# Kernel optimization log

Hardware: AMD Instinct MI355X
Metric: run time of the kernel (lower is better)

## Reference

```python
import jax, jax.numpy as jnp
import numpy as np


def setup_inputs() -> dict:
    key = jax.random.key(0)
    k1, k2, k3 = jax.random.split(key, 3)
    B, S, D, E, H = 4, 2048, 1024, 8, 1024
    x = jax.random.normal(k1, (B, S, D), dtype=jnp.float32)
    Wg = jax.random.normal(k2, (D, E), dtype=jnp.float32) / np.sqrt(D)
    We = jax.random.normal(k3, (E, D, H), dtype=jnp.float32) / np.sqrt(D)
    be = jnp.zeros((E, H), dtype=jnp.float32)
    return {"x": x, "Wg": Wg, "We": We, "be": be}


def reference(x, Wg, We, be):
    B, S, D = x.shape
    E = Wg.shape[1]
    T = B * S
    xf = x.reshape(T, D)
    # Top-2 gating (softmax over experts, renormalize the chosen 2)
    gates = jax.nn.softmax(xf @ Wg, axis=-1)                 # [T, E]
    top_g, top_i = jax.lax.top_k(gates, 2)                   # [T, 2]
    top_g = top_g / jnp.sum(top_g, axis=-1, keepdims=True)
    # Dense dispatch matrix: dispatch[e, t] = combined gate weight of token t for expert e
    tok = jnp.arange(T)
    dispatch = jnp.zeros((E, T), dtype=gates.dtype)
    for i in range(2):  # fixed top-2, not a data loop
        dispatch = dispatch.at[top_i[:, i], tok].add(top_g[:, i])
    # Per-expert linear (grouped GEMM over all tokens), then weighted combine
    y = jnp.einsum('td,edh->eth', xf, We) + be[:, None, :]   # [E, T, H]
    out = jnp.einsum('et,eth->th', dispatch, y)              # [T, H]
    return out.reshape(B, S, -1)
```

## Files before the change

### kernel.cpp

```cpp
#include <hip/hip_runtime.h>
#include <hip/hip_bf16.h>

#define T_TOK 8192
#define DDIM  1024
#define NEXP  8
#define HDIM  1024
#define SLOT_CAP 17536
#define NCBLK 32

typedef short bf16x8 __attribute__((ext_vector_type(8)));
typedef float f32x4  __attribute__((ext_vector_type(4)));

typedef const __attribute__((address_space(1))) unsigned int* gas_ptr;
typedef __attribute__((address_space(3))) unsigned int*       las_ptr;
#define GLD16(gp, lp) __builtin_amdgcn_global_load_lds((gas_ptr)(gp), (las_ptr)(lp), 16, 0, 0)

static __device__ __forceinline__ unsigned short f2b(float f) {
    union { float f; unsigned int u; } v; v.f = f;
    unsigned int u = v.u;
    u += 0x7fffu + ((u >> 16) & 1u);
    return (unsigned short)(u >> 16);
}
static __device__ __forceinline__ float b2f(unsigned short h) {
    union { unsigned int u; float f; } v; v.u = ((unsigned int)h) << 16;
    return v.f;
}

__global__ __launch_bounds__(256) void moe_routing(
    const float* __restrict__ x, const float* __restrict__ wg,
    unsigned short* __restrict__ xb,
    int* __restrict__ tok_e, float* __restrict__ tok_g)
{
    __shared__ double red[256 * 9];
    __shared__ double part[64];
    __shared__ double lf[NEXP];

    int t   = blockIdx.x;
    int tid = threadIdx.x;

    float4 xv = ((const float4*)(x + (size_t)t * DDIM))[tid];
    ushort4 xs;
    xs.x = f2b(xv.x); xs.y = f2b(xv.y); xs.z = f2b(xv.z); xs.w = f2b(xv.w);
    ((ushort4*)(xb + (size_t)t * DDIM))[tid] = xs;

    double s[NEXP];
    #pragma unroll
    for (int e = 0; e < NEXP; e++) s[e] = 0.0;
    const float* wr = wg + (size_t)tid * 4 * NEXP;
    #pragma unroll
    for (int j = 0; j < 4; j++) {
        double xj = (double)((&xv.x)[j]);
        #pragma unroll
        for (int e = 0; e < NEXP; e++)
            s[e] += xj * (double)wr[j * NEXP + e];
    }
    #pragma unroll
    for (int e = 0; e < NEXP; e++) red[tid * 9 + e] = s[e];
    __syncthreads();

    if (tid < 64) {
        int e = tid >> 3, p = tid & 7;
        double acc = 0.0;
        for (int i = 0; i < 32; i++) acc += red[(i * 8 + p) * 9 + e];
        part[tid] = acc;
    }
    __syncthreads();
    if (tid < NEXP) {
        double acc = 0.0;
        #pragma unroll
        for (int p = 0; p < 8; p++) acc += part[tid * 8 + p];
        lf[tid] = acc;
    }
    __syncthreads();

    if (tid == 0) {
        double l[NEXP];
        #pragma unroll
        for (int e = 0; e < NEXP; e++) l[e] = lf[e];
        int e0 = 0;
        for (int e = 1; e < NEXP; e++) if (l[e] > l[e0]) e0 = e;
        int e1 = (e0 == 0) ? 1 : 0;
        for (int e = 0; e < NEXP; e++) if (e != e0 && l[e] > l[e1]) e1 = e;
        double g0 = 1.0 / (1.0 + exp(l[e1] - l[e0]));
        double g1 = 1.0 - g0;
        tok_e[2*t] = e0; tok_e[2*t+1] = e1;
        tok_g[2*t] = (float)g0; tok_g[2*t+1] = (float)g1;
    }
}

__global__ __launch_bounds__(256) void moe_count(
    const int* __restrict__ tok_e, int* __restrict__ cnt_part)
{
    __shared__ int h[NEXP];
    if (threadIdx.x < NEXP) h[threadIdx.x] = 0;
    __syncthreads();
    int t = blockIdx.x * 256 + threadIdx.x;
    atomicAdd(&h[tok_e[2*t]], 1);
    atomicAdd(&h[tok_e[2*t+1]], 1);
    __syncthreads();
    if (threadIdx.x < NEXP)
        cnt_part[blockIdx.x * NEXP + threadIdx.x] = h[threadIdx.x];
}

__global__ void moe_offsets(const int* __restrict__ cnt_part,
                            int* __restrict__ meta, int* __restrict__ counts,
                            int* __restrict__ cursor) {
    __shared__ int c_s[NEXP];
    int tid = threadIdx.x;
    if (tid < NEXP) {
        int c = 0;
        for (int b = 0; b < NCBLK; b++) c += cnt_part[b * NEXP + tid];
        counts[tid] = c; c_s[tid] = c;
    }
    __syncthreads();
    if (tid == 0) {
        int off = 0;
        for (int e = 0; e < NEXP; e++) {
            meta[e] = off;
            cursor[e] = off;
            off += (c_s[e] + 127) & ~127;
        }
        meta[NEXP] = off;
    }
}

__global__ __launch_bounds__(256) void moe_slotfill(
    const int* __restrict__ tok_e, int* __restrict__ cursor,
    int* __restrict__ slot_token, int* __restrict__ tok_slot)
{
    __shared__ int h[NEXP];
    __shared__ int base[NEXP];
    if (threadIdx.x < NEXP) h[threadIdx.x] = 0;
    __syncthreads();
    int t = blockIdx.x * 256 + threadIdx.x;
    int e0 = tok_e[2*t],     e1 = tok_e[2*t + 1];
    int r0 = atomicAdd(&h[e0], 1);
    int r1 = atomicAdd(&h[e1], 1);
    __syncthreads();
    if (threadIdx.x < NEXP)
        base[threadIdx.x] = atomicAdd(&cursor[threadIdx.x], h[threadIdx.x]);
    __syncthreads();
    int s0 = base[e0] + r0, s1 = base[e1] + r1;
    slot_token[s0] = t;  tok_slot[2*t]     = s0;
    slot_token[s1] = t;  tok_slot[2*t + 1] = s1;
}

__global__ __launch_bounds__(256) void moe_wtrans(
    const float* __restrict__ we, unsigned short* __restrict__ wt)
{
    __shared__ unsigned short tile[64][65];
    int e  = blockIdx.z;
    int d0 = blockIdx.y * 64;
    int h0 = blockIdx.x * 64;
    int c  = threadIdx.x & 63;
    int r4 = threadIdx.x >> 6;
    #pragma unroll
    for (int i = 0; i < 64; i += 4)
        tile[r4 + i][c] = f2b(we[((size_t)e * DDIM + d0 + r4 + i) * HDIM + h0 + c]);
    __syncthreads();
    #pragma unroll
    for (int i = 0; i < 64; i += 4)
        wt[((size_t)e * HDIM + h0 + r4 + i) * DDIM + d0 + c] = tile[c][r4 + i];
}

__global__ __launch_bounds__(256, 4) void moe_gemm(
    const unsigned short* __restrict__ xb,
    const unsigned short* __restrict__ wt,
    const float* __restrict__ be,
    const int* __restrict__ slot_token,
    const int* __restrict__ meta,
    const int* __restrict__ counts,
    unsigned short* __restrict__ y_slot)
{
    __shared__ __align__(16) unsigned short As[3][128 * 32];
    __shared__ __align__(16) unsigned short Bs[2][128 * 32];

    int m0 = blockIdx.y * 128;
    if (m0 >= meta[NEXP]) return;
    int n0 = blockIdx.x * 128;

    int e = 0;
    #pragma unroll
    for (int i = 1; i < NEXP; i++) if (m0 >= meta[i]) e = i;
    int lim = meta[e] + counts[e];

    int tid  = threadIdx.x;
    int lane = tid & 63, wv = tid >> 6;

    int rA = 32 * wv + (lane >> 2);
    int kc = (((lane & 3) ^ ((rA >> 1) & 3)) * 8);
    int sA0 = m0 + rA, sA1 = sA0 + 16;
    int tA0 = (sA0 < lim) ? slot_token[sA0] : 0;
    int tA1 = (sA1 < lim) ? slot_token[sA1] : 0;
    const unsigned short* gA0 = xb + (size_t)tA0 * DDIM + kc;
    const unsigned short* gA1 = xb + (size_t)tA1 * DDIM + kc;
    const unsigned short* gB0 = wt + ((size_t)e * HDIM + n0 + rA) * DDIM + kc;
    const unsigned short* gB1 = gB0 + (size_t)16 * DDIM;
    int c0 = (2 * wv) * 512;
    int c1 = c0 + 512;

    f32x4 acc[4][4];
    #pragma unroll
    for (int i = 0; i < 4; i++)
        #pragma unroll
        for (int j = 0; j < 4; j++) acc[i][j] = (f32x4){0.f, 0.f, 0.f, 0.f};

    int wm = (wv >> 1) * 64, wn = (wv & 1) * 64;
    int l16 = lane & 15, quad = lane >> 4;
    int f = (l16 >> 1) & 3;
    int rdA[4], rdB[4];
    #pragma unroll
    for (int i = 0; i < 4; i++) {
        rdA[i] = (wm + i * 16 + l16) * 32 + ((quad ^ f) * 8);
        rdB[i] = (wn + i * 16 + l16) * 32 + ((quad ^ f) * 8);
    }

#define ISSUE_A(kkv, Ab)                                                      \
    {                                                                         \
        int ko = (kkv) * 32;                                                  \
        GLD16(gA0 + ko, (Ab) + c0);                                           \
        GLD16(gA1 + ko, (Ab) + c1);                                           \
    }
#define ISSUE_B(kkv, Bb)                                                      \
    {                                                                         \
        int ko = (kkv) * 32;                                                  \
        GLD16(gB0 + ko, (Bb) + c0);                                           \
        GLD16(gB1 + ko, (Bb) + c1);                                           \
    }
#define COMPUTE(Ab, Bb)                                                       \
    {                                                                         \
        bf16x8 bfr[4];                                                        \
        _Pragma("unroll")                                                     \
        for (int j = 0; j < 4; j++)                                           \
            bfr[j] = *(const bf16x8*)((Bb) + rdB[j]);                         \
        _Pragma("unroll")                                                     \
        for (int i = 0; i < 4; i++) {                                         \
            bf16x8 af = *(const bf16x8*)((Ab) + rdA[i]);                      \
            _Pragma("unroll")                                                 \
            for (int j = 0; j < 4; j++)                                       \
                acc[i][j] = __builtin_amdgcn_mfma_f32_16x16x32_bf16(          \
                    af, bfr[j], acc[i][j], 0, 0, 0);                          \
        }                                                                     \
    }

    unsigned short *A0 = As[0], *A1 = As[1], *A2 = As[2];
    unsigned short *B0 = Bs[0], *B1 = Bs[1];

    ISSUE_A(0, A0)
    ISSUE_B(0, B0)
    ISSUE_A(1, A1)

    #pragma unroll 1
    for (int kk = 0; kk < 32; ++kk) {
        asm volatile("" ::: "memory");
        if (kk == 31) __builtin_amdgcn_s_waitcnt(0x0F70);
        else          __builtin_amdgcn_s_waitcnt(0x0F72);
        __builtin_amdgcn_s_barrier();
        asm volatile("" ::: "memory");
        COMPUTE(A0, B0)
        if (kk < 31) ISSUE_B(kk + 1, B1)
        if (kk < 30) ISSUE_A(kk + 2, A2)
        unsigned short* tA = A0; A0 = A1; A1 = A2; A2 = tA;
        unsigned short* tB = B0; B0 = B1; B1 = tB;
    }
#undef ISSUE_A
#undef ISSUE_B
#undef COMPUTE

    #pragma unroll
    for (int i = 0; i < 4; i++) {
        #pragma unroll
        for (int r = 0; r < 4; r++) {
            int slot = m0 + wm + i * 16 + quad * 4 + r;
            if (slot >= lim) continue;
            unsigned short* yp = y_slot + (size_t)slot * HDIM + n0;
            #pragma unroll
            for (int j = 0; j < 4; j++) {
                int col = wn + j * 16 + l16;
                yp[col] = f2b(acc[i][j][r] + be[e * HDIM + n0 + col]);
            }
        }
    }
}

__global__ __launch_bounds__(256) void moe_combine(
    const unsigned short* __restrict__ y_slot,
    const int* __restrict__ tok_slot, const float* __restrict__ tok_g,
    float* __restrict__ out)
{
    int t   = blockIdx.x;
    int tid = threadIdx.x;
    int s0 = tok_slot[2 * t], s1 = tok_slot[2 * t + 1];
    float g0 = tok_g[2 * t],  g1 = tok_g[2 * t + 1];
    ushort4 a = ((const ushort4*)(y_slot + (size_t)s0 * HDIM))[tid];
    ushort4 b = ((const ushort4*)(y_slot + (size_t)s1 * HDIM))[tid];
    float4 o;
    o.x = g0 * b2f(a.x) + g1 * b2f(b.x);
    o.y = g0 * b2f(a.y) + g1 * b2f(b.y);
    o.z = g0 * b2f(a.z) + g1 * b2f(b.z);
    o.w = g0 * b2f(a.w) + g1 * b2f(b.w);
    ((float4*)(out + (size_t)t * HDIM))[tid] = o;
}

extern "C" void kernel_launch(void* const* d_in, const int* in_sizes, int n_in,
                              void* d_out, int out_size, void* d_ws, size_t ws_size,
                              hipStream_t stream) {
    const float* x  = (const float*)d_in[0];
    const float* wg = (const float*)d_in[1];
    const float* we = (const float*)d_in[2];
    const float* be = (const float*)d_in[3];
    float* out = (float*)d_out;

    char* ws = (char*)d_ws;
    size_t o = 0;
    auto alloc = [&](size_t bytes) -> void* {
        void* p = ws + o;
        o = (o + bytes + 255) & ~(size_t)255;
        return p;
    };
    unsigned short* xb   = (unsigned short*)alloc((size_t)T_TOK * DDIM * 2);
    unsigned short* wtb  = (unsigned short*)alloc((size_t)NEXP * HDIM * DDIM * 2);
    unsigned short* ysl  = (unsigned short*)alloc((size_t)SLOT_CAP * HDIM * 2);
    int*   slot_token    = (int*)  alloc((size_t)SLOT_CAP * 4);
    int*   cnt_part      = (int*)  alloc((size_t)NCBLK * NEXP * 4);
    int*   counts        = (int*)  alloc(NEXP * 4);
    int*   meta          = (int*)  alloc((NEXP + 1) * 4);
    int*   cursor        = (int*)  alloc(NEXP * 4);
    int*   tok_e         = (int*)  alloc((size_t)T_TOK * 2 * 4);
    float* tok_g         = (float*)alloc((size_t)T_TOK * 2 * 4);
    int*   tok_slot      = (int*)  alloc((size_t)T_TOK * 2 * 4);

    moe_routing<<<T_TOK, 256, 0, stream>>>(x, wg, xb, tok_e, tok_g);
    moe_count<<<NCBLK, 256, 0, stream>>>(tok_e, cnt_part);
    moe_offsets<<<1, 64, 0, stream>>>(cnt_part, meta, counts, cursor);
    moe_slotfill<<<NCBLK, 256, 0, stream>>>(tok_e, cursor, slot_token, tok_slot);
    moe_wtrans<<<dim3(HDIM / 64, DDIM / 64, NEXP), 256, 0, stream>>>(we, wtb);
    moe_gemm<<<dim3(HDIM / 128, SLOT_CAP / 128), 256, 0, stream>>>(
        xb, wtb, be, slot_token, meta, counts, ysl);
    moe_combine<<<T_TOK, 256, 0, stream>>>(ysl, tok_slot, tok_g, out);
}
```

Baseline: 220.3 us.

## Fuse offset computation into slotfill, remap GEMM block order, widen combine loads

Removes the single-block moe_offsets kernel: each slotfill block now computes the prefix offsets itself from the per-block counts, making slot assignment deterministic and saving one launch. The GEMM block index is remapped so that consecutive workgroups are spread across M tiles for the same N column group, which changes L2 reuse patterns. The combine kernel processes two tokens per block using 16-byte bf16 loads, halving its grid size. The gains from each piece are small and the GEMM remap could hurt or help cache locality.

```diff
diff --git a/kernel.cpp b/kernel.cpp
--- a/kernel.cpp
+++ b/kernel.cpp
@@ -10,6 +10,7 @@
 
 typedef short bf16x8 __attribute__((ext_vector_type(8)));
 typedef float f32x4  __attribute__((ext_vector_type(4)));
+typedef unsigned short u16x8 __attribute__((ext_vector_type(8)));
 
 typedef const __attribute__((address_space(1))) unsigned int* gas_ptr;
 typedef __attribute__((address_space(3))) unsigned int*       las_ptr;
@@ -102,43 +103,40 @@
         cnt_part[blockIdx.x * NEXP + threadIdx.x] = h[threadIdx.x];
 }
 
-__global__ void moe_offsets(const int* __restrict__ cnt_part,
-                            int* __restrict__ meta, int* __restrict__ counts,
-                            int* __restrict__ cursor) {
-    __shared__ int c_s[NEXP];
+__global__ __launch_bounds__(256) void moe_slotfill(
+    const int* __restrict__ tok_e, const int* __restrict__ cnt_part,
+    int* __restrict__ meta, int* __restrict__ counts,
+    int* __restrict__ slot_token, int* __restrict__ tok_slot)
+{
+    __shared__ int h[NEXP];
+    __shared__ int tots[NEXP], pres[NEXP], base[NEXP];
     int tid = threadIdx.x;
-    if (tid < NEXP) {
-        int c = 0;
-        for (int b = 0; b < NCBLK; b++) c += cnt_part[b * NEXP + tid];
-        counts[tid] = c; c_s[tid] = c;
-    }
-    __syncthreads();
-    if (tid == 0) {
-        int off = 0;
-        for (int e = 0; e < NEXP; e++) {
-            meta[e] = off;
-            cursor[e] = off;
-            off += (c_s[e] + 127) & ~127;
-        }
-        meta[NEXP] = off;
-    }
-}
-
-__global__ __launch_bounds__(256) void moe_slotfill(
-    const int* __restrict__ tok_e, int* __restrict__ cursor,
-    int* __restrict__ slot_token, int* __restrict__ tok_slot)
-{
-    __shared__ int h[NEXP];
-    __shared__ int base[NEXP];
-    if (threadIdx.x < NEXP) h[threadIdx.x] = 0;
-    __syncthreads();
-    int t = blockIdx.x * 256 + threadIdx.x;
+    if (tid < NEXP) h[tid] = 0;
+    __syncthreads();
+    int t = blockIdx.x * 256 + tid;
     int e0 = tok_e[2*t],     e1 = tok_e[2*t + 1];
     int r0 = atomicAdd(&h[e0], 1);
     int r1 = atomicAdd(&h[e1], 1);
-    __syncthreads();
-    if (threadIdx.x < NEXP)
-        base[threadIdx.x] = atomicAdd(&cursor[threadIdx.x], h[threadIdx.x]);
+    if (tid < NEXP) {
+        int pre = 0, tot = 0;
+        for (int b = 0; b < NCBLK; b++) {
+            int c = cnt_part[b * NEXP + tid];
+            if (b < (int)blockIdx.x) pre += c;
+            tot += c;
+        }
+        tots[tid] = tot; pres[tid] = pre;
+    }
+    __syncthreads();
+    if (tid < NEXP) {
+        int off = 0;
+        for (int e = 0; e < tid; e++) off += (tots[e] + 127) & ~127;
+        base[tid] = off + pres[tid];
+        if (blockIdx.x == 0) {
+            meta[tid]   = off;
+            counts[tid] = tots[tid];
+            if (tid == NEXP - 1) meta[NEXP] = off + ((tots[tid] + 127) & ~127);
+        }
+    }
     __syncthreads();
     int s0 = base[e0] + r0, s1 = base[e1] + r1;
     slot_token[s0] = t;  tok_slot[2*t]     = s0;
@@ -175,9 +173,11 @@
     __shared__ __align__(16) unsigned short As[3][128 * 32];
     __shared__ __align__(16) unsigned short Bs[2][128 * 32];
 
-    int m0 = blockIdx.y * 128;
+    int f   = blockIdx.y * gridDim.x + blockIdx.x;
+    int wid = (f & 7) * gridDim.y + (f >> 3);
+    int m0 = (wid >> 3) * 128;
     if (m0 >= meta[NEXP]) return;
-    int n0 = blockIdx.x * 128;
+    int n0 = (wid & 7) * 128;
 
     int e = 0;
     #pragma unroll
@@ -207,12 +207,12 @@
 
     int wm = (wv >> 1) * 64, wn = (wv & 1) * 64;
     int l16 = lane & 15, quad = lane >> 4;
-    int f = (l16 >> 1) & 3;
+    int ff = (l16 >> 1) & 3;
     int rdA[4], rdB[4];
     #pragma unroll
     for (int i = 0; i < 4; i++) {
-        rdA[i] = (wm + i * 16 + l16) * 32 + ((quad ^ f) * 8);
-        rdB[i] = (wn + i * 16 + l16) * 32 + ((quad ^ f) * 8);
+        rdA[i] = (wm + i * 16 + l16) * 32 + ((quad ^ ff) * 8);
+        rdB[i] = (wn + i * 16 + l16) * 32 + ((quad ^ ff) * 8);
     }
 
 #define ISSUE_A(kkv, Ab)                                                      \
@@ -288,18 +288,26 @@
     const int* __restrict__ tok_slot, const float* __restrict__ tok_g,
     float* __restrict__ out)
 {
-    int t   = blockIdx.x;
-    int tid = threadIdx.x;
+    int tid  = threadIdx.x;
+    int half = tid >> 7;
+    int lane = tid & 127;
+    int t = blockIdx.x * 2 + half;
     int s0 = tok_slot[2 * t], s1 = tok_slot[2 * t + 1];
     float g0 = tok_g[2 * t],  g1 = tok_g[2 * t + 1];
-    ushort4 a = ((const ushort4*)(y_slot + (size_t)s0 * HDIM))[tid];
-    ushort4 b = ((const ushort4*)(y_slot + (size_t)s1 * HDIM))[tid];
-    float4 o;
-    o.x = g0 * b2f(a.x) + g1 * b2f(b.x);
-    o.y = g0 * b2f(a.y) + g1 * b2f(b.y);
-    o.z = g0 * b2f(a.z) + g1 * b2f(b.z);
-    o.w = g0 * b2f(a.w) + g1 * b2f(b.w);
-    ((float4*)(out + (size_t)t * HDIM))[tid] = o;
+    u16x8 a = ((const u16x8*)(y_slot + (size_t)s0 * HDIM))[lane];
+    u16x8 b = ((const u16x8*)(y_slot + (size_t)s1 * HDIM))[lane];
+    float4 o0, o1;
+    o0.x = g0 * b2f(a[0]) + g1 * b2f(b[0]);
+    o0.y = g0 * b2f(a[1]) + g1 * b2f(b[1]);
+    o0.z = g0 * b2f(a[2]) + g1 * b2f(b[2]);
+    o0.w = g0 * b2f(a[3]) + g1 * b2f(b[3]);
+    o1.x = g0 * b2f(a[4]) + g1 * b2f(b[4]);
+    o1.y = g0 * b2f(a[5]) + g1 * b2f(b[5]);
+    o1.z = g0 * b2f(a[6]) + g1 * b2f(b[6]);
+    o1.w = g0 * b2f(a[7]) + g1 * b2f(b[7]);
+    float4* op = (float4*)(out + (size_t)t * HDIM) + lane * 2;
+    op[0] = o0;
+    op[1] = o1;
 }
 
 extern "C" void kernel_launch(void* const* d_in, const int* in_sizes, int n_in,
@@ -325,17 +333,16 @@
     int*   cnt_part      = (int*)  alloc((size_t)NCBLK * NEXP * 4);
     int*   counts        = (int*)  alloc(NEXP * 4);
     int*   meta          = (int*)  alloc((NEXP + 1) * 4);
-    int*   cursor        = (int*)  alloc(NEXP * 4);
     int*   tok_e         = (int*)  alloc((size_t)T_TOK * 2 * 4);
     float* tok_g         = (float*)alloc((size_t)T_TOK * 2 * 4);
     int*   tok_slot      = (int*)  alloc((size_t)T_TOK * 2 * 4);
 
     moe_routing<<<T_TOK, 256, 0, stream>>>(x, wg, xb, tok_e, tok_g);
     moe_count<<<NCBLK, 256, 0, stream>>>(tok_e, cnt_part);
-    moe_offsets<<<1, 64, 0, stream>>>(cnt_part, meta, counts, cursor);
-    moe_slotfill<<<NCBLK, 256, 0, stream>>>(tok_e, cursor, slot_token, tok_slot);
+    moe_slotfill<<<NCBLK, 256, 0, stream>>>(tok_e, cnt_part, meta, counts,
+                                            slot_token, tok_slot);
     moe_wtrans<<<dim3(HDIM / 64, DDIM / 64, NEXP), 256, 0, stream>>>(we, wtb);
     moe_gemm<<<dim3(HDIM / 128, SLOT_CAP / 128), 256, 0, stream>>>(
         xb, wtb, be, slot_token, meta, counts, ysl);
-    moe_combine<<<T_TOK, 256, 0, stream>>>(ysl, tok_slot, tok_g, out);
-}
+    moe_combine<<<T_TOK / 2, 256, 0, stream>>>(ysl, tok_slot, tok_g, out);
+}
```

Measured after the change: 216.2 us. No clear change (-1.9%).
